# Kernel tuning notes

Hardware: AMD Instinct MI355X
Metric: run time of the kernel (lower is better)

The kernel has to match this reference:

```python
import jax, jax.numpy as jnp
import numpy as np

NUM_CENTROID = 64
HIDDEN = 768
MAX_SEQ = 128
D = MAX_SEQ * HIDDEN  # 98304 flattened feature dim
NUM_ITERS = 10        # fixed Lloyd iterations (original loops to tol; fixed for jit)


def _cdist(x, c):
    x2 = jnp.sum(x * x, axis=-1, keepdims=True)          # [N,1]
    c2 = jnp.sum(c * c, axis=-1)                          # [K]
    d2 = x2 + c2[None, :] - 2.0 * (x @ c.T)               # [N,K]
    return jnp.sqrt(jnp.maximum(d2, 0.0))


def setup_inputs() -> dict:
    key = jax.random.key(0)
    k1, k2 = jax.random.split(key)
    x = jax.random.normal(k1, (1024, MAX_SEQ, HIDDEN), dtype=jnp.float32)
    # centroid table initialized as Normal(mean=0.07, std=0.39) per the module
    centroid = 0.07 + 0.39 * jax.random.normal(k2, (NUM_CENTROID, D), dtype=jnp.float32)
    return {"x": x, "centroid": centroid}


def reference(x, centroid):
    X = x.reshape(-1, D)                                  # [N, D]
    N = X.shape[0]
    # 'resuming' branch: snap each centroid to its nearest sample
    dis0 = _cdist(X, centroid)                            # [N, K]
    choice_points = jnp.argmin(dis0, axis=0)              # [K]
    state = X[choice_points]                              # [K, D]
    ones = jnp.ones((N,), dtype=X.dtype)

    def step(state, _):
        dis = _cdist(X, state)                            # [N, K]
        choice = jnp.argmin(dis, axis=1)                  # [N]
        sums = jax.ops.segment_sum(X, choice, num_segments=NUM_CENTROID)   # [K, D]
        counts = jax.ops.segment_sum(ones, choice, num_segments=NUM_CENTROID)  # [K]
        nonempty = counts[:, None] > 0
        new_state = jnp.where(nonempty, sums / jnp.maximum(counts[:, None], 1.0), state)
        return new_state, choice

    state, choices = jax.lax.scan(step, state, None, length=NUM_ITERS)
    # returns (new centroids, final cluster assignments) like the module
    return state, choices[-1]
```

## Files before the change

### kernel.cpp

```cpp
#include <hip/hip_runtime.h>
#include <cstddef>
#include <cstdint>


#define N_PTS  1024
#define K_C    64
#define D_DIM  98304
#define ITERS  10
#define SPLITD 64
#define BM     64
#define DC     64
#define LDSP   72
#define NCHK   96
#define CCHK   12
#define NGRP   32
#define SHPG   6
#define SHW    512
#define NCHT   96
#define NPAIR  36
#define GT     128
#define GDC    32

typedef __attribute__((ext_vector_type(8))) short bf16x8;
typedef __attribute__((ext_vector_type(8))) unsigned short ushort8;
typedef __attribute__((ext_vector_type(4))) float f32x4;

__device__ __forceinline__ unsigned short f2bf(float x) {
    unsigned u = __float_as_uint(x);
    u = (u + 0x7FFFu + ((u >> 16) & 1u)) >> 16;
    return (unsigned short)u;
}
__device__ __forceinline__ float bf2f(unsigned short b) {
    return __uint_as_float((unsigned)b << 16);
}
__device__ __forceinline__ void cvt2(float x, unsigned short& h, unsigned short& l) {
    h = f2bf(x);
    l = f2bf(x - bf2f(h));
}

__device__ __forceinline__ void gload_lds16(const unsigned short* g, char* l) {
    __builtin_amdgcn_global_load_lds(
        (const __attribute__((address_space(1))) unsigned int*)g,
        (__attribute__((address_space(3))) unsigned int*)l, 16, 0, 0);
}

__device__ __forceinline__ float block_sum256(float s) {
    #pragma unroll
    for (int o = 32; o; o >>= 1) s += __shfl_down(s, o);
    __shared__ float red[4];
    int lane = threadIdx.x & 63, w = threadIdx.x >> 6;
    if (lane == 0) red[w] = s;
    __syncthreads();
    return red[0] + red[1] + red[2] + red[3];
}

__global__ __launch_bounds__(256) void convert_kernel(const float* __restrict__ A,
                                                      unsigned short* __restrict__ Ph,
                                                      unsigned short* __restrict__ Pl,
                                                      float* __restrict__ sq_part) {
    const int n = blockIdx.x, j = blockIdx.y;
    const size_t base = (size_t)n * D_DIM + (size_t)j * 8192;
    const int t = threadIdx.x;
    float ss = 0.f;
    #pragma unroll
    for (int i = 0; i < 4; ++i) {
        size_t e = base + (size_t)i * 2048 + t * 8;
        float4 a = *reinterpret_cast<const float4*>(A + e);
        float4 b = *reinterpret_cast<const float4*>(A + e + 4);
        ss += a.x*a.x + a.y*a.y + a.z*a.z + a.w*a.w;
        ss += b.x*b.x + b.y*b.y + b.z*b.z + b.w*b.w;
        ushort4 h0, l0, h1, l1;
        cvt2(a.x, h0.x, l0.x); cvt2(a.y, h0.y, l0.y);
        cvt2(a.z, h0.z, l0.z); cvt2(a.w, h0.w, l0.w);
        cvt2(b.x, h1.x, l1.x); cvt2(b.y, h1.y, l1.y);
        cvt2(b.z, h1.z, l1.z); cvt2(b.w, h1.w, l1.w);
        *reinterpret_cast<ushort4*>(Ph + e)     = h0;
        *reinterpret_cast<ushort4*>(Ph + e + 4) = h1;
        *reinterpret_cast<ushort4*>(Pl + e)     = l0;
        *reinterpret_cast<ushort4*>(Pl + e + 4) = l1;
    }
    ss = block_sum256(ss);
    if (t == 0) sq_part[n * CCHK + j] = ss;
}

__global__ __launch_bounds__(256) void reduce_sq_kernel(const float* __restrict__ sq_part,
                                                        float* __restrict__ out, int rows) {
    int n = blockIdx.x * 256 + threadIdx.x;
    if (n >= rows) return;
    float s = 0.f;
    #pragma unroll
    for (int j = 0; j < CCHK; ++j) s += sq_part[n * CCHK + j];
    out[n] = s;
}

__global__ __launch_bounds__(256) void mfma_dot_kernel(const unsigned short* __restrict__ Xh,
                                                       const unsigned short* __restrict__ Xl,
                                                       const unsigned short* __restrict__ Sh,
                                                       const unsigned short* __restrict__ Sl,
                                                       float* __restrict__ partial) {
    __shared__ alignas(16) short Bh[K_C][LDSP];
    __shared__ alignas(16) short Bl[K_C][LDSP];

    const int seg = blockIdx.x, nblk = blockIdx.y;
    const int t = threadIdx.x;
    const int wid = t >> 6, lane = t & 63;
    const int d_begin = seg * (D_DIM / SPLITD);
    const int NCH = (D_DIM / SPLITD) / DC;

    const int arow = nblk * BM + wid * 16 + (lane & 15);
    const int ko = (lane >> 4) * 8;
    const unsigned short* xh = Xh + (size_t)arow * D_DIM;
    const unsigned short* xl = Xl + (size_t)arow * D_DIM;

    const int sr = t >> 2, sc = (t & 3) * 16;
    const unsigned short* shp = Sh + (size_t)sr * D_DIM;
    const unsigned short* slp = Sl + (size_t)sr * D_DIM;

    ushort8 s0, s1, s2, s3;
    bf16x8 aEh0, aEh1, aEl0, aEl1;
    bf16x8 aOh0, aOh1, aOl0, aOl1;

    auto loadB = [&](int d0) {
        s0 = *reinterpret_cast<const ushort8*>(shp + d0 + sc);
        s1 = *reinterpret_cast<const ushort8*>(shp + d0 + sc + 8);
        s2 = *reinterpret_cast<const ushort8*>(slp + d0 + sc);
        s3 = *reinterpret_cast<const ushort8*>(slp + d0 + sc + 8);
    };
    auto storeB = [&]() {
        *reinterpret_cast<ushort8*>(&Bh[sr][sc])     = s0;
        *reinterpret_cast<ushort8*>(&Bh[sr][sc + 8]) = s1;
        *reinterpret_cast<ushort8*>(&Bl[sr][sc])     = s2;
        *reinterpret_cast<ushort8*>(&Bl[sr][sc + 8]) = s3;
    };

    f32x4 acc[4];
    #pragma unroll
    for (int i = 0; i < 4; ++i) acc[i] = f32x4{0.f, 0.f, 0.f, 0.f};

    #define LOADA(bh0, bh1, bl0, bl1, d0)                                        \
        bh0 = *reinterpret_cast<const bf16x8*>(xh + (d0) + ko);                  \
        bh1 = *reinterpret_cast<const bf16x8*>(xh + (d0) + 32 + ko);             \
        bl0 = *reinterpret_cast<const bf16x8*>(xl + (d0) + ko);                  \
        bl1 = *reinterpret_cast<const bf16x8*>(xl + (d0) + 32 + ko);

    #define MFMAS(ah0, ah1, al0, al1)                                            \
        _Pragma("unroll")                                                        \
        for (int nb = 0; nb < 4; ++nb) {                                         \
            const int br = nb * 16 + (lane & 15);                                \
            bf16x8 bh = *reinterpret_cast<const bf16x8*>(&Bh[br][ko]);           \
            bf16x8 bl = *reinterpret_cast<const bf16x8*>(&Bl[br][ko]);           \
            acc[nb] = __builtin_amdgcn_mfma_f32_16x16x32_bf16(ah0, bh, acc[nb], 0, 0, 0); \
            acc[nb] = __builtin_amdgcn_mfma_f32_16x16x32_bf16(ah0, bl, acc[nb], 0, 0, 0); \
            acc[nb] = __builtin_amdgcn_mfma_f32_16x16x32_bf16(al0, bh, acc[nb], 0, 0, 0); \
        }                                                                        \
        _Pragma("unroll")                                                        \
        for (int nb = 0; nb < 4; ++nb) {                                         \
            const int br = nb * 16 + (lane & 15);                                \
            bf16x8 bh = *reinterpret_cast<const bf16x8*>(&Bh[br][32 + ko]);      \
            bf16x8 bl = *reinterpret_cast<const bf16x8*>(&Bl[br][32 + ko]);      \
            acc[nb] = __builtin_amdgcn_mfma_f32_16x16x32_bf16(ah1, bh, acc[nb], 0, 0, 0); \
            acc[nb] = __builtin_amdgcn_mfma_f32_16x16x32_bf16(ah1, bl, acc[nb], 0, 0, 0); \
            acc[nb] = __builtin_amdgcn_mfma_f32_16x16x32_bf16(al1, bh, acc[nb], 0, 0, 0); \
        }

    loadB(d_begin);
    LOADA(aEh0, aEh1, aEl0, aEl1, d_begin);
    for (int c = 0; c < NCH; c += 2) {
        __syncthreads();
        storeB();
        __syncthreads();
        {
            int dn = d_begin + (c + 1) * DC;
            loadB(dn);
            LOADA(aOh0, aOh1, aOl0, aOl1, dn);
        }
        MFMAS(aEh0, aEh1, aEl0, aEl1);
        __syncthreads();
        storeB();
        __syncthreads();
        if (c + 2 < NCH) {
            int dn = d_begin + (c + 2) * DC;
            loadB(dn);
            LOADA(aEh0, aEh1, aEl0, aEl1, dn);
        }
        MFMAS(aOh0, aOh1, aOl0, aOl1);
    }
    #undef LOADA
    #undef MFMAS

    #pragma unroll
    for (int nb = 0; nb < 4; ++nb)
        #pragma unroll
        for (int r = 0; r < 4; ++r) {
            int row = wid * 16 + (lane >> 4) * 4 + r;
            int col = nb * 16 + (lane & 15);
            int n = nblk * BM + row;
            partial[((size_t)seg * N_PTS + n) * K_C + col] = acc[nb][r];
        }
}

__global__ __launch_bounds__(256) void reduce_dot_kernel(const float* __restrict__ partial,
                                                         float* __restrict__ dot) {
    int i = blockIdx.x * 256 + threadIdx.x;
    float s = 0.f;
    #pragma unroll 8
    for (int p = 0; p < SPLITD; ++p) s += partial[(size_t)p * N_PTS * K_C + i];
    dot[i] = s;
}

__global__ __launch_bounds__(256) void argmin_n_kernel(const float* __restrict__ dot,
                                                       const float* __restrict__ x2,
                                                       int* __restrict__ choice_pts) {
    int k = blockIdx.x;
    float best = 3.4e38f; int bi = N_PTS;
    for (int n = threadIdx.x; n < N_PTS; n += 256) {
        float v = fmaf(-2.f, dot[n * K_C + k], x2[n]);
        if (v < best || (v == best && n < bi)) { best = v; bi = n; }
    }
    #pragma unroll
    for (int off = 32; off; off >>= 1) {
        float v2 = __shfl_down(best, off);
        int   i2 = __shfl_down(bi, off);
        if (v2 < best || (v2 == best && i2 < bi)) { best = v2; bi = i2; }
    }
    __shared__ float bv[4]; __shared__ int bix[4];
    int lane = threadIdx.x & 63, wid = threadIdx.x >> 6;
    if (lane == 0) { bv[wid] = best; bix[wid] = bi; }
    __syncthreads();
    if (threadIdx.x == 0) {
        for (int w = 1; w < 4; ++w)
            if (bv[w] < best || (bv[w] == best && bix[w] < bi)) { best = bv[w]; bi = bix[w]; }
        choice_pts[k] = bi;
    }
}

__global__ __launch_bounds__(256) void gather_kernel(const float* __restrict__ X,
                                                     const int* __restrict__ choice_pts,
                                                     float* __restrict__ state) {
    int k = blockIdx.x;
    int c = choice_pts[k];
    size_t d = (size_t)blockIdx.y * 1024 + threadIdx.x * 4;
    float4 v = *reinterpret_cast<const float4*>(X + (size_t)c * D_DIM + d);
    *reinterpret_cast<float4*>(state + (size_t)k * D_DIM + d) = v;
}

__global__ __launch_bounds__(256, 3) void gbuild_kernel(const unsigned short* __restrict__ Xh,
                                                        const unsigned short* __restrict__ Xl,
                                                        float* __restrict__ Gpart) {
    __shared__ alignas(16) char LA[16384];
    __shared__ alignas(16) char LB[16384];

    const int id = blockIdx.x;
    const int xr = id & 7, q = id >> 3;
    const int p = q % NPAIR;
    const int g = ((q / NPAIR) << 3) + xr;
    int bi = 0, rem = p, rl = 8;
    while (rem >= rl) { rem -= rl; --rl; ++bi; }
    const int bj = bi + rem;

    const int t = threadIdx.x;
    const int wid = t >> 6, lane = t & 63;
    const int wr = wid >> 1, wc = wid & 1;

    const int isA = (wid < 2) ? 1 : 0;
    const int i0 = (wid & 1) * 8;
    char* ltile = isA ? LA : LB;
    const int rowbase = (isA ? bi : bj) * GT;
    const int lw = (lane & 7) ^ (lane >> 3);
    const unsigned short* plane = (lw & 4) ? Xl : Xh;
    const unsigned short* gbase[8];
    #pragma unroll
    for (int j = 0; j < 8; ++j)
        gbase[j] = plane + (size_t)(rowbase + (i0 + j) * 8 + (lane >> 3)) * D_DIM + (lw & 3) * 8;

    const int sh = (lane >> 4) ^ (lane & 7);
    const int sl = (4 + (lane >> 4)) ^ (lane & 7);
    const int ra0 = (wr * 64 + (lane & 15)) * 128;
    const int rb0 = (wc * 64 + (lane & 15)) * 128;

    f32x4 acc[4][4];
    #pragma unroll
    for (int i = 0; i < 4; ++i)
        #pragma unroll
        for (int j = 0; j < 4; ++j) acc[i][j] = f32x4{0.f, 0.f, 0.f, 0.f};

    for (int idx = 0; idx < NCHT; ++idx) {
        const int d0 = (g + ((idx >> 4) << 5)) * SHW + (idx & 15) * GDC;
        __syncthreads();
        #pragma unroll
        for (int j = 0; j < 8; ++j)
            gload_lds16(gbase[j] + d0, ltile + (i0 + j) * 1024);
        __syncthreads();
        bf16x8 ah[4], al[4];
        #pragma unroll
        for (int fi = 0; fi < 4; ++fi) {
            ah[fi] = *reinterpret_cast<const bf16x8*>(LA + ra0 + fi * 2048 + sh * 16);
            al[fi] = *reinterpret_cast<const bf16x8*>(LA + ra0 + fi * 2048 + sl * 16);
        }
        #pragma unroll
        for (int fj = 0; fj < 4; ++fj) {
            bf16x8 bh = *reinterpret_cast<const bf16x8*>(LB + rb0 + fj * 2048 + sh * 16);
            bf16x8 bl = *reinterpret_cast<const bf16x8*>(LB + rb0 + fj * 2048 + sl * 16);
            #pragma unroll
            for (int fi = 0; fi < 4; ++fi) {
                acc[fi][fj] = __builtin_amdgcn_mfma_f32_16x16x32_bf16(ah[fi], bh, acc[fi][fj], 0, 0, 0);
                acc[fi][fj] = __builtin_amdgcn_mfma_f32_16x16x32_bf16(ah[fi], bl, acc[fi][fj], 0, 0, 0);
                acc[fi][fj] = __builtin_amdgcn_mfma_f32_16x16x32_bf16(al[fi], bh, acc[fi][fj], 0, 0, 0);
            }
        }
    }

    float* gp = Gpart + ((size_t)g * NPAIR + p) * (GT * GT);
    #pragma unroll
    for (int fi = 0; fi < 4; ++fi)
        #pragma unroll
        for (int fj = 0; fj < 4; ++fj)
            #pragma unroll
            for (int r2 = 0; r2 < 4; ++r2) {
                int row = wr * 64 + fi * 16 + (lane >> 4) * 4 + r2;
                int col = wc * 64 + fj * 16 + (lane & 15);
                gp[row * GT + col] = acc[fi][fj][r2];
            }
}

__global__ __launch_bounds__(256) void reduce_g_kernel(const float* __restrict__ Gpart,
                                                       float* __restrict__ G) {
    const int p = blockIdx.x, blk = blockIdx.y;
    int bi = 0, rem = p, rl = 8;
    while (rem >= rl) { rem -= rl; --rl; ++bi; }
    const int bj = bi + rem;
    const int e0 = blk * 1024 + threadIdx.x * 4;
    float sx = 0.f, sy = 0.f, sz = 0.f, sw = 0.f;
    #pragma unroll 8
    for (int g = 0; g < NGRP; ++g) {
        const float4 v = *reinterpret_cast<const float4*>(
            Gpart + ((size_t)g * NPAIR + p) * (GT * GT) + e0);
        sx += v.x; sy += v.y; sz += v.z; sw += v.w;
    }
    const int row = e0 >> 7, col = e0 & 127;
    const int gi = bi * GT + row, gj = bj * GT + col;
    float4 o = {sx, sy, sz, sw};
    *reinterpret_cast<float4*>(&G[(size_t)gi * N_PTS + gj]) = o;
    if (bi != bj) {
        G[(size_t)(gj + 0) * N_PTS + gi] = sx;
        G[(size_t)(gj + 1) * N_PTS + gi] = sy;
        G[(size_t)(gj + 2) * N_PTS + gi] = sz;
        G[(size_t)(gj + 3) * N_PTS + gi] = sw;
    }
}

__global__ __launch_bounds__(256) void dot0_kernel(const float* __restrict__ G,
                                                   const int* __restrict__ cpts,
                                                   const float* __restrict__ x2,
                                                   float* __restrict__ dot,
                                                   float* __restrict__ c2) {
    int g = blockIdx.x * 256 + threadIdx.x;
    int n = g >> 6, k = g & 63;
    dot[g] = G[(size_t)n * N_PTS + cpts[k]];
    if (g < K_C) c2[g] = x2[cpts[g]];
}

__global__ __launch_bounds__(256) void assign_g_kernel(const float* __restrict__ dot,
                                                       const float* __restrict__ c2,
                                                       int* __restrict__ choice_it) {
    int wid = threadIdx.x >> 6, lane = threadIdx.x & 63;
    int n = blockIdx.x * 4 + wid;
    float v = fmaf(-2.f, dot[n * K_C + lane], c2[lane]);
    int bi = lane;
    #pragma unroll
    for (int m = 32; m; m >>= 1) {
        float v2 = __shfl_xor(v, m);
        int   i2 = __shfl_xor(bi, m);
        if (v2 < v || (v2 == v && i2 < bi)) { v = v2; bi = i2; }
    }
    if (lane == 0) choice_it[n] = bi;
}

__global__ __launch_bounds__(1024) void sort2_kernel(const int* __restrict__ choice,
                                                     int* __restrict__ order,
                                                     int* __restrict__ cstart,
                                                     int* __restrict__ tlast,
                                                     int it) {
    __shared__ int ch[N_PTS];
    __shared__ int cnt[K_C];
    __shared__ int cst[K_C + 1];
    int t = threadIdx.x;
    if (t < K_C) cnt[t] = 0;
    __syncthreads();
    int c = choice[t];
    ch[t] = c;
    atomicAdd(&cnt[c], 1);
    __syncthreads();
    if (t == 0) {
        int a = 0;
        for (int k = 0; k < K_C; ++k) { cst[k] = a; a += cnt[k]; }
        cst[K_C] = a;
    }
    __syncthreads();
    if (t <= K_C) cstart[t] = cst[t];
    if (t < K_C && cnt[t] > 0) tlast[t] = it;
    int r = 0;
    for (int m = 0; m < t; ++m) r += (ch[m] == c);
    order[cst[c] + r] = t;
}

__global__ __launch_bounds__(256) void dotup_kernel(const float* __restrict__ G,
                                                    const int* __restrict__ order,
                                                    const int* __restrict__ cstart,
                                                    float* __restrict__ dot) {
    __shared__ int ord[N_PTS];
    __shared__ int cst[K_C + 1];
    int t = threadIdx.x;
    #pragma unroll
    for (int i = 0; i < 4; ++i) ord[t + 256 * i] = order[t + 256 * i];
    if (t <= K_C) cst[t] = cstart[t];
    __syncthreads();
    int wid = t >> 6, lane = t & 63;
    int n = blockIdx.x * 4 + wid;
    int b = cst[lane], e = cst[lane + 1];
    if (b == e) return;
    const float* gr = G + (size_t)n * N_PTS;
    float s = 0.f;
    for (int i = b; i < e; ++i) s += gr[ord[i]];
    dot[n * K_C + lane] = s / (float)(e - b);
}

__global__ __launch_bounds__(64) void c2up_kernel(const float* __restrict__ dot,
                                                  const int* __restrict__ order,
                                                  const int* __restrict__ cstart,
                                                  float* __restrict__ c2) {
    int k = threadIdx.x;
    int b = cstart[k], e = cstart[k + 1];
    if (b == e) return;
    float s = 0.f;
    for (int i = b; i < e; ++i) s += dot[order[i] * K_C + k];
    c2[k] = s / (float)(e - b);
}

__global__ __launch_bounds__(64) void init_tlast_kernel(int* __restrict__ tlast) {
    tlast[threadIdx.x] = -1;
}

__global__ __launch_bounds__(256) void final_state_kernel(const float* __restrict__ X,
                                                          const int* __restrict__ chbuf,
                                                          const int* __restrict__ tlast,
                                                          float* __restrict__ state) {
    const int k = blockIdx.x;
    const int tk = tlast[k];
    if (tk < 0) return;
    __shared__ int chs[N_PTS];
    const int* src = chbuf + tk * N_PTS;
    const int t = threadIdx.x;
    #pragma unroll
    for (int i = 0; i < 4; ++i) chs[t + 256 * i] = src[t + 256 * i];
    __syncthreads();
    const size_t d = (size_t)blockIdx.y * 1024 + t * 4;
    float sx = 0.f, sy = 0.f, sz = 0.f, sw = 0.f;
    int cm = 0;
    for (int n = 0; n < N_PTS; ++n) {
        if (chs[n] == k) {
            ++cm;
            const float4 v = *reinterpret_cast<const float4*>(X + (size_t)n * D_DIM + d);
            sx += v.x; sy += v.y; sz += v.z; sw += v.w;
        }
    }
    float inv = 1.f / (float)cm;
    float4 o = {sx * inv, sy * inv, sz * inv, sw * inv};
    *reinterpret_cast<float4*>(state + (size_t)k * D_DIM + d) = o;
}

__global__ __launch_bounds__(256) void choice_out_kernel(const int* __restrict__ choice,
                                                         float* __restrict__ out) {
    int n = blockIdx.x * 256 + threadIdx.x;
    if (n < N_PTS) out[n] = (float)choice[n];
}

extern "C" void kernel_launch(void* const* d_in, const int* in_sizes, int n_in,
                              void* d_out, int out_size, void* d_ws, size_t ws_size,
                              hipStream_t stream) {
    const float* X  = (const float*)d_in[0];
    const float* C0 = (const float*)d_in[1];
    float* state      = (float*)d_out;
    float* out_choice = state + (size_t)K_C * D_DIM;

    char* w = (char*)d_ws;
    size_t off = 0;
    auto alloc = [&](size_t bytes) { void* p = w + off; off = (off + bytes + 255) & ~(size_t)255; return p; };
    unsigned short* Xh = (unsigned short*)alloc((size_t)N_PTS * D_DIM * 2);
    unsigned short* Xl = (unsigned short*)alloc((size_t)N_PTS * D_DIM * 2);
    unsigned short* Sh = (unsigned short*)alloc((size_t)K_C * D_DIM * 2);
    unsigned short* Sl = (unsigned short*)alloc((size_t)K_C * D_DIM * 2);
    float* partial = (float*)alloc((size_t)SPLITD * N_PTS * K_C * 4);
    float* Gpart   = (float*)alloc((size_t)NGRP * NPAIR * GT * GT * 4);
    float* G       = (float*)alloc((size_t)N_PTS * N_PTS * 4);
    float* dotb    = (float*)alloc((size_t)N_PTS * K_C * 4);
    float* x2p     = (float*)alloc((size_t)N_PTS * CCHK * 4);
    float* x2      = (float*)alloc((size_t)N_PTS * 4);
    float* c0sq    = (float*)alloc((size_t)K_C * CCHK * 4);
    float* dotg    = (float*)alloc((size_t)N_PTS * K_C * 4);
    float* c2      = (float*)alloc(256);
    int* cpts      = (int*)alloc(256);
    int* chbuf     = (int*)alloc((size_t)ITERS * N_PTS * 4);
    int* order     = (int*)alloc((size_t)N_PTS * 4);
    int* cstart    = (int*)alloc(512);
    int* tlast     = (int*)alloc(256);

    dim3 b256(256);

    convert_kernel<<<dim3(N_PTS, CCHK), b256, 0, stream>>>(X, Xh, Xl, x2p);
    reduce_sq_kernel<<<dim3(4), b256, 0, stream>>>(x2p, x2, N_PTS);

    gbuild_kernel<<<dim3(8 * NPAIR * (NGRP / 8)), b256, 0, stream>>>(Xh, Xl, Gpart);
    reduce_g_kernel<<<dim3(NPAIR, 16), b256, 0, stream>>>(Gpart, G);

    convert_kernel<<<dim3(K_C, CCHK), b256, 0, stream>>>(C0, Sh, Sl, c0sq);
    mfma_dot_kernel<<<dim3(SPLITD, N_PTS / BM), b256, 0, stream>>>(Xh, Xl, Sh, Sl, partial);
    reduce_dot_kernel<<<dim3(N_PTS * K_C / 256), b256, 0, stream>>>(partial, dotb);
    argmin_n_kernel<<<K_C, b256, 0, stream>>>(dotb, x2, cpts);
    gather_kernel<<<dim3(K_C, NCHK), b256, 0, stream>>>(X, cpts, state);
    init_tlast_kernel<<<1, dim3(64), 0, stream>>>(tlast);
    dot0_kernel<<<dim3(N_PTS * K_C / 256), b256, 0, stream>>>(G, cpts, x2, dotg, c2);

    for (int it = 0; it < ITERS; ++it) {
        assign_g_kernel<<<dim3(N_PTS / 4), b256, 0, stream>>>(dotg, c2, chbuf + it * N_PTS);
        sort2_kernel<<<1, dim3(1024), 0, stream>>>(chbuf + it * N_PTS, order, cstart, tlast, it);
        if (it < ITERS - 1) {
            dotup_kernel<<<dim3(N_PTS / 4), b256, 0, stream>>>(G, order, cstart, dotg);
            c2up_kernel<<<1, dim3(64), 0, stream>>>(dotg, order, cstart, c2);
        }
    }

    final_state_kernel<<<dim3(K_C, NCHK), b256, 0, stream>>>(X, chbuf, tlast, state);
    choice_out_kernel<<<dim3(N_PTS / 256), b256, 0, stream>>>(chbuf + (ITERS - 1) * N_PTS, out_choice);
}
```

Measured before the change: 1.928 ms.

## Double-buffer LDS tiles in Gram build and halve split-D groups

Gives the gbuild kernel's LDS two ping-pong stages so the next chunk's global-to-LDS loads are issued before the current chunk's MFMAs, with explicit vmcnt waits and barriers in place of syncthreads. This is meant to overlap memory latency with the split-bf16 matrix math. It also halves the number of D-split groups (NGRP 32→16) and doubles the chunks per block, which reduces partial Gram writes and reduce work but launches fewer blocks. LDS use grows to 64KB and occupancy drops from 3 to 2 blocks per CU.

Measured after the change: 1.898 ms. About the same (-1.6%).

```diff
diff --git a/kernel.cpp b/kernel.cpp
--- a/kernel.cpp
+++ b/kernel.cpp
@@ -13,10 +13,10 @@
 #define LDSP   72
 #define NCHK   96
 #define CCHK   12
-#define NGRP   32
-#define SHPG   6
+#define NGRP   16
+#define SHPG   12
 #define SHW    512
-#define NCHT   96
+#define NCHT   192
 #define NPAIR  36
 #define GT     128
 #define GDC    32
@@ -244,11 +244,10 @@
     *reinterpret_cast<float4*>(state + (size_t)k * D_DIM + d) = v;
 }
 
-__global__ __launch_bounds__(256, 3) void gbuild_kernel(const unsigned short* __restrict__ Xh,
+__global__ __launch_bounds__(256, 2) void gbuild_kernel(const unsigned short* __restrict__ Xh,
                                                         const unsigned short* __restrict__ Xl,
                                                         float* __restrict__ Gpart) {
-    __shared__ alignas(16) char LA[16384];
-    __shared__ alignas(16) char LB[16384];
+    __shared__ alignas(16) char L[65536];
 
     const int id = blockIdx.x;
     const int xr = id & 7, q = id >> 3;
@@ -264,7 +263,7 @@
 
     const int isA = (wid < 2) ? 1 : 0;
     const int i0 = (wid & 1) * 8;
-    char* ltile = isA ? LA : LB;
+    const int tileoff = isA ? 0 : 16384;
     const int rowbase = (isA ? bi : bj) * GT;
     const int lw = (lane & 7) ^ (lane >> 3);
     const unsigned short* plane = (lw & 4) ? Xl : Xh;
@@ -276,7 +275,7 @@
     const int sh = (lane >> 4) ^ (lane & 7);
     const int sl = (4 + (lane >> 4)) ^ (lane & 7);
     const int ra0 = (wr * 64 + (lane & 15)) * 128;
-    const int rb0 = (wc * 64 + (lane & 15)) * 128;
+    const int rb0 = 16384 + (wc * 64 + (lane & 15)) * 128;
 
     f32x4 acc[4][4];
     #pragma unroll
@@ -284,23 +283,35 @@
         #pragma unroll
         for (int j = 0; j < 4; ++j) acc[i][j] = f32x4{0.f, 0.f, 0.f, 0.f};
 
-    for (int idx = 0; idx < NCHT; ++idx) {
-        const int d0 = (g + ((idx >> 4) << 5)) * SHW + (idx & 15) * GDC;
-        __syncthreads();
+    auto issue = [&](int idx) {
+        const int d0 = (g + ((idx >> 4) << 4)) * SHW + (idx & 15) * GDC;
+        char* dst = L + ((idx & 1) << 15) + tileoff + i0 * 1024;
         #pragma unroll
         for (int j = 0; j < 8; ++j)
-            gload_lds16(gbase[j] + d0, ltile + (i0 + j) * 1024);
-        __syncthreads();
+            gload_lds16(gbase[j] + d0, dst + j * 1024);
+    };
+
+    issue(0);
+    for (int idx = 0; idx < NCHT; ++idx) {
+        if (idx + 1 < NCHT) {
+            issue(idx + 1);
+            asm volatile("s_waitcnt vmcnt(8)" ::: "memory");
+        } else {
+            asm volatile("s_waitcnt vmcnt(0)" ::: "memory");
+        }
+        __builtin_amdgcn_s_barrier();
+        __builtin_amdgcn_sched_barrier(0);
+        const char* base = L + ((idx & 1) << 15);
         bf16x8 ah[4], al[4];
         #pragma unroll
         for (int fi = 0; fi < 4; ++fi) {
-            ah[fi] = *reinterpret_cast<const bf16x8*>(LA + ra0 + fi * 2048 + sh * 16);
-            al[fi] = *reinterpret_cast<const bf16x8*>(LA + ra0 + fi * 2048 + sl * 16);
+            ah[fi] = *reinterpret_cast<const bf16x8*>(base + ra0 + fi * 2048 + sh * 16);
+            al[fi] = *reinterpret_cast<const bf16x8*>(base + ra0 + fi * 2048 + sl * 16);
         }
         #pragma unroll
         for (int fj = 0; fj < 4; ++fj) {
-            bf16x8 bh = *reinterpret_cast<const bf16x8*>(LB + rb0 + fj * 2048 + sh * 16);
-            bf16x8 bl = *reinterpret_cast<const bf16x8*>(LB + rb0 + fj * 2048 + sl * 16);
+            bf16x8 bh = *reinterpret_cast<const bf16x8*>(base + rb0 + fj * 2048 + sh * 16);
+            bf16x8 bl = *reinterpret_cast<const bf16x8*>(base + rb0 + fj * 2048 + sl * 16);
             #pragma unroll
             for (int fi = 0; fi < 4; ++fi) {
                 acc[fi][fj] = __builtin_amdgcn_mfma_f32_16x16x32_bf16(ah[fi], bh, acc[fi][fj], 0, 0, 0);
@@ -308,6 +319,8 @@
                 acc[fi][fj] = __builtin_amdgcn_mfma_f32_16x16x32_bf16(al[fi], bh, acc[fi][fj], 0, 0, 0);
             }
         }
+        __builtin_amdgcn_sched_barrier(0);
+        __builtin_amdgcn_s_barrier();
     }
 
     float* gp = Gpart + ((size_t)g * NPAIR + p) * (GT * GT);
```
